# Performance work log

Hardware: AMD Instinct MI355X
Metric: run time of the kernel (lower is better)

Reference implementation:

```python
import jax, jax.numpy as jnp
from jax import lax
import numpy as np

L, QD, B = 16, 2048, 4096


def setup_inputs() -> dict:
    key = jax.random.key(0)
    k1, k2, k3, k4 = jax.random.split(key, 4)
    input_state = jax.random.normal(k1, (B, QD), dtype=jnp.float32)
    # rotation_angles ~ U(-0.1, 0.1) per _initialize_parameters
    rotation_angles = jax.random.uniform(k2, (L, QD, 3), dtype=jnp.float32, minval=-0.1, maxval=0.1)
    # xavier_uniform for [qd, qd] weights: bound = sqrt(6 / (qd + qd))
    bound = float(np.sqrt(6.0 / (QD + QD)))
    entanglement_weights = jax.random.uniform(k3, (L, QD, QD), dtype=jnp.float32, minval=-bound, maxval=bound)
    # orthogonal init for measurement basis via QR
    m = jax.random.normal(k4, (QD, QD), dtype=jnp.float32)
    q, r = jnp.linalg.qr(m)
    measurement_basis = (q * jnp.sign(jnp.diagonal(r))).astype(jnp.float32)
    return {
        "input_state": input_state,
        "rotation_angles": rotation_angles,
        "entanglement_weights": entanglement_weights,
        "measurement_basis": measurement_basis,
    }


def reference(input_state, rotation_angles, entanglement_weights, measurement_basis):
    # Each rotation gate reduces to an elementwise scale by cos(angle/2):
    #   x-gate: real(rot[0,0]) = cos(a/2); y-gate: cos(a/2); z-gate: real(exp(-i a/2)) = cos(a/2).
    # Fuse all three gates per layer into one per-dim scale: [L, QD]
    scales = jnp.prod(jnp.cos(rotation_angles * 0.5), axis=-1)

    def layer_step(state, layer_params):
        scale, w = layer_params  # scale: [QD], w: [QD, QD]
        return jnp.matmul(state * scale, w), None

    state, _ = lax.scan(layer_step, input_state, (scales, entanglement_weights))
    return jnp.matmul(state, measurement_basis)
```

## Files before the change

### kernel.cpp

```cpp
#include <hip/hip_runtime.h>
#include <stdint.h>

#define L_LAYERS 16
#define QD 2048
#define BATCH 4096

typedef __attribute__((ext_vector_type(8))) __bf16 bf16x8;
typedef __attribute__((ext_vector_type(4))) float f32x4;
typedef __attribute__((address_space(3))) uint32_t lds32_t;
typedef const __attribute__((address_space(1))) uint32_t glob32_t;

__device__ __forceinline__ void async_load16(const void* g, void* l) {
    __builtin_amdgcn_global_load_lds((glob32_t*)(uintptr_t)g, (lds32_t*)(uintptr_t)l,
                                     16, 0, 0);
}

__device__ __forceinline__ unsigned short f2bf(float f) {
    uint32_t u = __float_as_uint(f);
    u += 0x7FFFu + ((u >> 16) & 1u);
    return (unsigned short)(u >> 16);
}

__global__ void scales_kernel(const float* __restrict__ ang, float* __restrict__ sc, int n) {
    int i = blockIdx.x * 256 + threadIdx.x;
    if (i < n) {
        float a0 = ang[3 * i + 0], a1 = ang[3 * i + 1], a2 = ang[3 * i + 2];
        sc[i] = __cosf(a0 * 0.5f) * __cosf(a1 * 0.5f) * __cosf(a2 * 0.5f);
    }
}

__global__ void convert_in_kernel(const float* __restrict__ in,
                                  unsigned short* __restrict__ out, int n4) {
    int i = blockIdx.x * 256 + threadIdx.x;
    if (i < n4) {
        float4 v = ((const float4*)in)[i];
        ushort4 o;
        o.x = f2bf(v.x); o.y = f2bf(v.y); o.z = f2bf(v.z); o.w = f2bf(v.w);
        ((ushort4*)out)[i] = o;
    }
}

__global__ void convert_a_all(const float* __restrict__ W, const float* __restrict__ sc,
                              unsigned short* __restrict__ out) {
    const int z = blockIdx.z;
    const float* src = W + (size_t)(2 * z) * QD * QD;
    const float* srow = sc + (2 * z) * QD;
    unsigned short* dst = out + (size_t)z * QD * QD;
    int i = blockIdx.x * 256 + threadIdx.x;
    float s = srow[i >> 9];
    float4 v = ((const float4*)src)[i];
    ushort4 o;
    o.x = f2bf(v.x * s); o.y = f2bf(v.y * s); o.z = f2bf(v.z * s); o.w = f2bf(v.w * s);
    ((ushort4*)dst)[i] = o;
}

__device__ __forceinline__ void conv_tile_body(const float* __restrict__ src,
                                               const float* __restrict__ srow,
                                               unsigned short* __restrict__ dst) {
    __shared__ __align__(16) unsigned short tile[64][72];
    const int t = threadIdx.x;
    const int k0 = blockIdx.y * 64, n0 = blockIdx.x * 64;
    const int r = t >> 4;
    const int c = (t & 15) * 4;
#pragma unroll
    for (int rr = 0; rr < 64; rr += 16) {
        int k = k0 + r + rr;
        float s = srow ? srow[k] : 1.0f;
        float4 v = *(const float4*)(src + (size_t)k * QD + n0 + c);
        tile[c + 0][r + rr] = f2bf(v.x * s);
        tile[c + 1][r + rr] = f2bf(v.y * s);
        tile[c + 2][r + rr] = f2bf(v.z * s);
        tile[c + 3][r + rr] = f2bf(v.w * s);
    }
    __syncthreads();
    const int wr = t >> 3;
    const int wc = (t & 7) * 8;
#pragma unroll
    for (int rr = 0; rr < 64; rr += 32) {
        *(float4*)(dst + (size_t)(n0 + wr + rr) * QD + k0 + wc) =
            *(const float4*)(&tile[wr + rr][wc]);
    }
}

__global__ void convert_b_all(const float* __restrict__ W, const float* __restrict__ Mb,
                              const float* __restrict__ sc, unsigned short* __restrict__ out) {
    const int z = blockIdx.z;
    const float* src = (z < 8) ? (W + (size_t)(2 * z + 1) * QD * QD) : Mb;
    const float* srow = (z < 8) ? (sc + (2 * z + 1) * QD) : nullptr;
    unsigned short* dst = out + (size_t)z * QD * QD;
    conv_tile_body(src, srow, dst);
}

struct GemmBatch {
    const unsigned short* a[8];
    const unsigned short* b[8];
    void* c[8];
};

template <int OUT_BF16, int TM>
__global__ __launch_bounds__(256, TM == 128 ? 2 : 4)
void gemm_kernel(GemmBatch args) {
    constexpr int NI = TM / 32;
    __shared__ __align__(16) unsigned short ldsA[TM * 64];
    __shared__ __align__(16) unsigned short ldsB[128 * 64];
    const unsigned short* __restrict__ A  = args.a[blockIdx.z];
    const unsigned short* __restrict__ Bt = args.b[blockIdx.z];
    void* __restrict__ Cout = args.c[blockIdx.z];

    const int t = threadIdx.x;
    const int n0 = blockIdx.x * 128;
    const int m0 = blockIdx.y * TM;
    const int lane = t & 63;
    const int wave = t >> 6;
    const int wm = (wave & 1) * (TM / 2);
    const int wn = (wave >> 1) * 64;
    const int fr = lane & 15;
    const int quad = lane >> 4;

    f32x4 acc[NI][4] = {};

    const int sr = t >> 2;
    const int scol = (t & 3) * 8;
    const unsigned short* ga = A + (size_t)(m0 + sr) * QD + scol;
    const unsigned short* gb = Bt + (size_t)(n0 + sr) * QD + scol;
    unsigned short* la = ldsA + t * 8;
    unsigned short* lb = ldsB + t * 8;

    for (int k0 = 0; k0 < QD; k0 += 64) {
        __syncthreads();
        if constexpr (TM == 128) {
            async_load16(ga, la);
            async_load16(ga + 64 * QD, la + 2048);
            async_load16(ga + 32, la + 4096);
            async_load16(ga + 32 + 64 * QD, la + 6144);
        } else {
            async_load16(ga, la);
            async_load16(ga + 32, la + 2048);
        }
        async_load16(gb, lb);
        async_load16(gb + 64 * QD, lb + 2048);
        async_load16(gb + 32, lb + 4096);
        async_load16(gb + 32 + 64 * QD, lb + 6144);
        ga += 64;
        gb += 64;
        __syncthreads();

#pragma unroll
        for (int kk = 0; kk < 2; kk++) {
            const unsigned short* pa = ldsA + kk * (TM * 32);
            const unsigned short* pb = ldsB + kk * 4096;
            bf16x8 af[NI], bfr[4];
#pragma unroll
            for (int i = 0; i < NI; i++)
                af[i] = *(const bf16x8*)(pa + (wm + i * 16 + fr) * 32 + quad * 8);
#pragma unroll
            for (int j = 0; j < 4; j++)
                bfr[j] = *(const bf16x8*)(pb + (wn + j * 16 + fr) * 32 + quad * 8);
#pragma unroll
            for (int i = 0; i < NI; i++)
#pragma unroll
                for (int j = 0; j < 4; j++)
                    acc[i][j] = __builtin_amdgcn_mfma_f32_16x16x32_bf16(af[i], bfr[j],
                                                                        acc[i][j], 0, 0, 0);
        }
    }

#pragma unroll
    for (int i = 0; i < NI; i++) {
        const int gr = m0 + wm + i * 16 + quad * 4;
#pragma unroll
        for (int j = 0; j < 4; j++) {
            const int gc = n0 + wn + j * 16 + fr;
#pragma unroll
            for (int r = 0; r < 4; r++) {
                float v = acc[i][j][r];
                if (OUT_BF16)
                    ((unsigned short*)Cout)[(size_t)(gr + r) * QD + gc] = f2bf(v);
                else
                    ((float*)Cout)[(size_t)(gr + r) * QD + gc] = v;
            }
        }
    }
}

__device__ __forceinline__ void stage_half(const unsigned short* __restrict__ G,
                                           int row0, int k0,
                                           unsigned char* dst, int t) {
    const int r = t >> 3;
    const int c = 8 * ((t & 7) ^ (r & 7));
    const unsigned short* g = G + (size_t)(row0 + r) * QD + k0 + c;
    async_load16(g, dst + t * 16);
    async_load16(g + 64 * QD, dst + 8192 + t * 16);
}

template <int OUT_BF16>
__global__ __launch_bounds__(512, 2)
void gemm256_kernel(GemmBatch args) {
    __shared__ __align__(16) unsigned char lds[131072];
    const unsigned short* __restrict__ A  = args.a[blockIdx.z];
    const unsigned short* __restrict__ Bt = args.b[blockIdx.z];
    void* __restrict__ Cout = args.c[blockIdx.z];

    const int t = threadIdx.x;
    const int lane = t & 63;
    const int wid = t >> 6;
    const int wm = (wid >> 2) * 128;
    const int wn = (wid & 3) * 64;
    const int fr = lane & 15;
    const int quad = lane >> 4;
    const int m0 = blockIdx.y * 256;
    const int n0 = blockIdx.x * 256;

    unsigned char* ldsA8 = lds;
    unsigned char* ldsB8 = lds + 65536;
    const int swz45 = (fr & 3) << 4;
    const int frb2 = (fr >> 2) & 1;
    const int kof0 = frb2 << 6;
    const int kof1 = (frb2 ^ 1) << 6;
    const unsigned char* sA = ldsA8 + (wm >> 7) * 16384 + fr * 128 + ((quad * 16) ^ swz45);
    const unsigned char* sB = ldsB8 + ((wn >> 7) & 1) * 16384 + (wn & 64) * 128
                              + fr * 128 + ((quad * 16) ^ swz45);

    f32x4 acc[8][4] = {};
    bf16x8 af[4][2], bfA[2][2], bfB[2][2];

    constexpr int NT = QD / 64;

    stage_half(A,  m0,       0,  ldsA8,         t);
    stage_half(A,  m0 + 128, 0,  ldsA8 + 16384, t);
    stage_half(Bt, n0,       0,  ldsB8,         t);
    stage_half(Bt, n0 + 128, 0,  ldsB8 + 16384, t);
    stage_half(A,  m0,       64, ldsA8 + 32768, t);
    stage_half(Bt, n0,       64, ldsB8 + 32768, t);
    asm volatile("s_waitcnt vmcnt(4)" ::: "memory");
    __builtin_amdgcn_s_barrier();

    for (int kt = 0; kt < NT; ++kt) {
        const int buf  = (kt & 1) << 15;
        const int nbuf = (~kt & 1) << 15;
        const int k1 = ((kt + 1) & (NT - 1)) << 6;
        const int k2 = ((kt + 2) & (NT - 1)) << 6;

#pragma unroll
        for (int mf = 0; mf < 4; mf++)
#pragma unroll
            for (int kk = 0; kk < 2; kk++)
                af[mf][kk] = *(const bf16x8*)(sA + buf + mf * 2048 + (kk ? kof1 : kof0));
#pragma unroll
        for (int nf = 0; nf < 2; nf++)
#pragma unroll
            for (int kk = 0; kk < 2; kk++)
                bfA[nf][kk] = *(const bf16x8*)(sB + buf + nf * 2048 + (kk ? kof1 : kof0));
        stage_half(A, m0 + 128, k1, ldsA8 + nbuf + 16384, t);
        __builtin_amdgcn_s_barrier();
        __builtin_amdgcn_s_setprio(1);
#pragma unroll
        for (int mf = 0; mf < 4; mf++)
#pragma unroll
            for (int nf = 0; nf < 2; nf++)
#pragma unroll
                for (int kk = 0; kk < 2; kk++)
                    acc[mf][nf] = __builtin_amdgcn_mfma_f32_16x16x32_bf16(
                        af[mf][kk], bfA[nf][kk], acc[mf][nf], 0, 0, 0);
        __builtin_amdgcn_s_setprio(0);
        __builtin_amdgcn_s_barrier();

#pragma unroll
        for (int nf = 0; nf < 2; nf++)
#pragma unroll
            for (int kk = 0; kk < 2; kk++)
                bfB[nf][kk] = *(const bf16x8*)(sB + buf + (nf + 2) * 2048 + (kk ? kof1 : kof0));
        stage_half(Bt, n0 + 128, k1, ldsB8 + nbuf + 16384, t);
        __builtin_amdgcn_s_barrier();
        __builtin_amdgcn_s_setprio(1);
#pragma unroll
        for (int mf = 0; mf < 4; mf++)
#pragma unroll
            for (int nf = 0; nf < 2; nf++)
#pragma unroll
                for (int kk = 0; kk < 2; kk++)
                    acc[mf][nf + 2] = __builtin_amdgcn_mfma_f32_16x16x32_bf16(
                        af[mf][kk], bfB[nf][kk], acc[mf][nf + 2], 0, 0, 0);
        __builtin_amdgcn_s_setprio(0);
        __builtin_amdgcn_s_barrier();

#pragma unroll
        for (int mf = 0; mf < 4; mf++)
#pragma unroll
            for (int kk = 0; kk < 2; kk++)
                af[mf][kk] = *(const bf16x8*)(sA + buf + (mf + 4) * 2048 + (kk ? kof1 : kof0));
        stage_half(Bt, n0, k2, ldsB8 + buf, t);
        __builtin_amdgcn_s_barrier();
        __builtin_amdgcn_s_setprio(1);
#pragma unroll
        for (int mf = 0; mf < 4; mf++)
#pragma unroll
            for (int nf = 0; nf < 2; nf++)
#pragma unroll
                for (int kk = 0; kk < 2; kk++)
                    acc[mf + 4][nf + 2] = __builtin_amdgcn_mfma_f32_16x16x32_bf16(
                        af[mf][kk], bfB[nf][kk], acc[mf + 4][nf + 2], 0, 0, 0);
        __builtin_amdgcn_s_setprio(0);
        __builtin_amdgcn_s_barrier();

        stage_half(A, m0, k2, ldsA8 + buf, t);
        __builtin_amdgcn_s_barrier();
        __builtin_amdgcn_s_setprio(1);
#pragma unroll
        for (int mf = 0; mf < 4; mf++)
#pragma unroll
            for (int nf = 0; nf < 2; nf++)
#pragma unroll
                for (int kk = 0; kk < 2; kk++)
                    acc[mf + 4][nf] = __builtin_amdgcn_mfma_f32_16x16x32_bf16(
                        af[mf][kk], bfA[nf][kk], acc[mf + 4][nf], 0, 0, 0);
        __builtin_amdgcn_s_setprio(0);
        asm volatile("s_waitcnt vmcnt(4)" ::: "memory");
        __builtin_amdgcn_s_barrier();
    }

    asm volatile("s_waitcnt vmcnt(0)" ::: "memory");

#pragma unroll
    for (int mf = 0; mf < 8; mf++) {
        const int gr = m0 + wm + mf * 16 + quad * 4;
#pragma unroll
        for (int nf = 0; nf < 4; nf++) {
            const int gc = n0 + wn + nf * 16 + fr;
#pragma unroll
            for (int r = 0; r < 4; r++) {
                float v = acc[mf][nf][r];
                if (OUT_BF16)
                    ((unsigned short*)Cout)[(size_t)(gr + r) * QD + gc] = f2bf(v);
                else
                    ((float*)Cout)[(size_t)(gr + r) * QD + gc] = v;
            }
        }
    }
}

extern "C" void kernel_launch(void* const* d_in, const int* in_sizes, int n_in,
                              void* d_out, int out_size, void* d_ws, size_t ws_size,
                              hipStream_t stream) {
    const float* input_state = (const float*)d_in[0];
    const float* angles      = (const float*)d_in[1];
    const float* W           = (const float*)d_in[2];
    const float* Mb          = (const float*)d_in[3];

    const size_t mat = (size_t)QD * QD;
    char* ws = (char*)d_ws;
    float* scales = (float*)ws;
    size_t off = 131072;
    unsigned short* xb = (unsigned short*)(ws + off); off += (size_t)BATCH * QD * 2;
    unsigned short* WA = (unsigned short*)(ws + off); off += 8 * mat * 2;
    unsigned short* WB = (unsigned short*)(ws + off); off += 9 * mat * 2;
    unsigned short* T1 = (unsigned short*)(ws + off); off += 8 * mat * 2;
    unsigned short* T2 = (unsigned short*)(ws + off); off += 4 * mat * 2;
    unsigned short* T3 = (unsigned short*)(ws + off); off += 2 * mat * 2;
    unsigned short* T4 = (unsigned short*)(ws + off); off += mat * 2;
    unsigned short* T5 = (unsigned short*)(ws + off); off += mat * 2;

    scales_kernel<<<(L_LAYERS * QD + 255) / 256, 256, 0, stream>>>(angles, scales,
                                                                   L_LAYERS * QD);
    convert_in_kernel<<<(BATCH * QD / 4) / 256, 256, 0, stream>>>(input_state, xb,
                                                                  BATCH * QD / 4);
    convert_a_all<<<dim3(mat / 4 / 256, 1, 8), 256, 0, stream>>>(W, scales, WA);
    convert_b_all<<<dim3(QD / 64, QD / 64, 9), 256, 0, stream>>>(W, Mb, scales, WB);

    GemmBatch b1{};
    for (int i = 0; i < 8; i++) {
        const unsigned short* wa = WA + (size_t)i * mat;
        const unsigned short* wb = WB + (size_t)i * mat;
        if ((i & 1) == 0) { b1.a[i] = wa; b1.b[i] = wb; }
        else              { b1.a[i] = wb; b1.b[i] = wa; }
        b1.c[i] = T1 + (size_t)i * mat;
    }
    gemm256_kernel<1><<<dim3(QD / 256, QD / 256, 8), 512, 0, stream>>>(b1);

    GemmBatch b2{};
    for (int i = 0; i < 4; i++) {
        b2.a[i] = T1 + (size_t)(2 * i + (i & 1)) * mat;
        b2.b[i] = T1 + (size_t)(2 * i + 1 - (i & 1)) * mat;
        b2.c[i] = T2 + (size_t)i * mat;
    }
    gemm256_kernel<1><<<dim3(QD / 256, QD / 256, 4), 512, 0, stream>>>(b2);

    GemmBatch b3{};
    for (int i = 0; i < 2; i++) {
        b3.a[i] = T2 + (size_t)(2 * i + (i & 1)) * mat;
        b3.b[i] = T2 + (size_t)(2 * i + 1 - (i & 1)) * mat;
        b3.c[i] = T3 + (size_t)i * mat;
    }
    gemm_kernel<1, 128><<<dim3(QD / 128, QD / 128, 2), 256, 0, stream>>>(b3);

    GemmBatch b4{};
    b4.a[0] = T3; b4.b[0] = T3 + mat; b4.c[0] = T4;
    gemm_kernel<1, 64><<<dim3(QD / 128, QD / 64, 1), 256, 0, stream>>>(b4);

    GemmBatch b5{};
    b5.a[0] = WB + 8 * mat; b5.b[0] = T4; b5.c[0] = T5;
    gemm_kernel<1, 64><<<dim3(QD / 128, QD / 64, 1), 256, 0, stream>>>(b5);

    GemmBatch ba{};
    ba.a[0] = xb; ba.b[0] = T5; ba.c[0] = d_out;
    gemm_kernel<0, 128><<<dim3(QD / 128, BATCH / 128, 1), 256, 0, stream>>>(ba);
}
```

Measured before the change: 744.7 us.

## Fuse scale computation into converters, swizzle transpose LDS, remap GEMM block order

Drops the separate scales kernel and recomputes the per-row cosine scale inline inside both weight-conversion kernels, removing one launch and a small buffer round trip. The transpose tile in the B converter now uses an XOR swizzle instead of padding, so LDS writes and reads avoid bank conflicts. The 256x256 GEMM kernel remaps the linear block index so consecutive workgroups are spread across batched matrices and tiles, aiming for better cache and channel spread. Recomputing the cosines per element adds redundant transcendental work in the converters.

Measured after the change: 733.3 us. No clear change (-1.5%).

```diff
diff --git a/kernel.cpp b/kernel.cpp
--- a/kernel.cpp
+++ b/kernel.cpp
@@ -21,12 +21,10 @@
     return (unsigned short)(u >> 16);
 }
 
-__global__ void scales_kernel(const float* __restrict__ ang, float* __restrict__ sc, int n) {
-    int i = blockIdx.x * 256 + threadIdx.x;
-    if (i < n) {
-        float a0 = ang[3 * i + 0], a1 = ang[3 * i + 1], a2 = ang[3 * i + 2];
-        sc[i] = __cosf(a0 * 0.5f) * __cosf(a1 * 0.5f) * __cosf(a2 * 0.5f);
-    }
+__device__ __forceinline__ float layer_scale(const float* __restrict__ ang,
+                                             int lay, int k) {
+    const float* ap = ang + ((size_t)lay * QD + k) * 3;
+    return __cosf(ap[0] * 0.5f) * __cosf(ap[1] * 0.5f) * __cosf(ap[2] * 0.5f);
 }
 
 __global__ void convert_in_kernel(const float* __restrict__ in,
@@ -40,14 +38,13 @@
     }
 }
 
-__global__ void convert_a_all(const float* __restrict__ W, const float* __restrict__ sc,
+__global__ void convert_a_all(const float* __restrict__ W, const float* __restrict__ ang,
                               unsigned short* __restrict__ out) {
     const int z = blockIdx.z;
     const float* src = W + (size_t)(2 * z) * QD * QD;
-    const float* srow = sc + (2 * z) * QD;
     unsigned short* dst = out + (size_t)z * QD * QD;
     int i = blockIdx.x * 256 + threadIdx.x;
-    float s = srow[i >> 9];
+    float s = layer_scale(ang, 2 * z, i >> 9);
     float4 v = ((const float4*)src)[i];
     ushort4 o;
     o.x = f2bf(v.x * s); o.y = f2bf(v.y * s); o.z = f2bf(v.z * s); o.w = f2bf(v.w * s);
@@ -55,40 +52,45 @@
 }
 
 __device__ __forceinline__ void conv_tile_body(const float* __restrict__ src,
-                                               const float* __restrict__ srow,
+                                               const float* __restrict__ ang,
+                                               int lay,
                                                unsigned short* __restrict__ dst) {
-    __shared__ __align__(16) unsigned short tile[64][72];
+    __shared__ __align__(16) unsigned short tile[64][64];
     const int t = threadIdx.x;
     const int k0 = blockIdx.y * 64, n0 = blockIdx.x * 64;
     const int r = t >> 4;
     const int c = (t & 15) * 4;
+    const int g = (t & 7) << 3;
 #pragma unroll
     for (int rr = 0; rr < 64; rr += 16) {
         int k = k0 + r + rr;
-        float s = srow ? srow[k] : 1.0f;
+        float s = (lay >= 0) ? layer_scale(ang, lay, k) : 1.0f;
         float4 v = *(const float4*)(src + (size_t)k * QD + n0 + c);
-        tile[c + 0][r + rr] = f2bf(v.x * s);
-        tile[c + 1][r + rr] = f2bf(v.y * s);
-        tile[c + 2][r + rr] = f2bf(v.z * s);
-        tile[c + 3][r + rr] = f2bf(v.w * s);
+        int col = (r + rr) ^ g;
+        tile[c + 0][col] = f2bf(v.x * s);
+        tile[c + 1][col] = f2bf(v.y * s);
+        tile[c + 2][col] = f2bf(v.z * s);
+        tile[c + 3][col] = f2bf(v.w * s);
     }
     __syncthreads();
     const int wr = t >> 3;
     const int wc = (t & 7) * 8;
 #pragma unroll
     for (int rr = 0; rr < 64; rr += 32) {
-        *(float4*)(dst + (size_t)(n0 + wr + rr) * QD + k0 + wc) =
-            *(const float4*)(&tile[wr + rr][wc]);
+        int row = wr + rr;
+        int pc = wc ^ (((row >> 2) & 7) << 3);
+        *(float4*)(dst + (size_t)(n0 + row) * QD + k0 + wc) =
+            *(const float4*)(&tile[row][pc]);
     }
 }
 
 __global__ void convert_b_all(const float* __restrict__ W, const float* __restrict__ Mb,
-                              const float* __restrict__ sc, unsigned short* __restrict__ out) {
+                              const float* __restrict__ ang, unsigned short* __restrict__ out) {
     const int z = blockIdx.z;
     const float* src = (z < 8) ? (W + (size_t)(2 * z + 1) * QD * QD) : Mb;
-    const float* srow = (z < 8) ? (sc + (2 * z + 1) * QD) : nullptr;
+    const int lay = (z < 8) ? (2 * z + 1) : -1;
     unsigned short* dst = out + (size_t)z * QD * QD;
-    conv_tile_body(src, srow, dst);
+    conv_tile_body(src, ang, lay, dst);
 }
 
 struct GemmBatch {
@@ -197,9 +199,15 @@
 __global__ __launch_bounds__(512, 2)
 void gemm256_kernel(GemmBatch args) {
     __shared__ __align__(16) unsigned char lds[131072];
-    const unsigned short* __restrict__ A  = args.a[blockIdx.z];
-    const unsigned short* __restrict__ Bt = args.b[blockIdx.z];
-    void* __restrict__ Cout = args.c[blockIdx.z];
+
+    const int lin = blockIdx.x + ((blockIdx.y + (blockIdx.z << 3)) << 3);
+    const int cpx = gridDim.z << 3;
+    const int m = (lin & 7) * cpx + (lin >> 3);
+    const int bx = m & 7, by = (m >> 3) & 7, bz = m >> 6;
+
+    const unsigned short* __restrict__ A  = args.a[bz];
+    const unsigned short* __restrict__ Bt = args.b[bz];
+    void* __restrict__ Cout = args.c[bz];
 
     const int t = threadIdx.x;
     const int lane = t & 63;
@@ -208,8 +216,8 @@
     const int wn = (wid & 3) * 64;
     const int fr = lane & 15;
     const int quad = lane >> 4;
-    const int m0 = blockIdx.y * 256;
-    const int n0 = blockIdx.x * 256;
+    const int m0 = by * 256;
+    const int n0 = bx * 256;
 
     unsigned char* ldsA8 = lds;
     unsigned char* ldsB8 = lds + 65536;
@@ -349,7 +357,6 @@
 
     const size_t mat = (size_t)QD * QD;
     char* ws = (char*)d_ws;
-    float* scales = (float*)ws;
     size_t off = 131072;
     unsigned short* xb = (unsigned short*)(ws + off); off += (size_t)BATCH * QD * 2;
     unsigned short* WA = (unsigned short*)(ws + off); off += 8 * mat * 2;
@@ -360,12 +367,10 @@
     unsigned short* T4 = (unsigned short*)(ws + off); off += mat * 2;
     unsigned short* T5 = (unsigned short*)(ws + off); off += mat * 2;
 
-    scales_kernel<<<(L_LAYERS * QD + 255) / 256, 256, 0, stream>>>(angles, scales,
-                                                                   L_LAYERS * QD);
     convert_in_kernel<<<(BATCH * QD / 4) / 256, 256, 0, stream>>>(input_state, xb,
                                                                   BATCH * QD / 4);
-    convert_a_all<<<dim3(mat / 4 / 256, 1, 8), 256, 0, stream>>>(W, scales, WA);
-    convert_b_all<<<dim3(QD / 64, QD / 64, 9), 256, 0, stream>>>(W, Mb, scales, WB);
+    convert_a_all<<<dim3(mat / 4 / 256, 1, 8), 256, 0, stream>>>(W, angles, WA);
+    convert_b_all<<<dim3(QD / 64, QD / 64, 9), 256, 0, stream>>>(W, Mb, angles, WB);
 
     GemmBatch b1{};
     for (int i = 0; i < 8; i++) {
```
